# Performance work log

Measured on AMD Instinct MI355X. Metric: run time of the kernel, lower is better.

The kernel has to match this reference:

```python
import jax, jax.numpy as jnp
import numpy as np

N, L, LEADS = 512, 640, 3
COND_DIM, NUM_K, DIM_K = 1, 100, 5
FLAT = 256 * 79  # 20224, from conv stack trace


def _leaky(x):
    return jnp.where(x >= 0, x, 0.2 * x)


def _sn(w, u):
    # PyTorch spectral_norm: one power iteration (u, v detached), sigma = u^T W v
    wm = w.reshape(w.shape[0], -1)
    v = wm.T @ u
    v = v / (jnp.linalg.norm(v) + 1e-12)
    u2 = wm @ v
    u2 = u2 / (jnp.linalg.norm(u2) + 1e-12)
    u2 = jax.lax.stop_gradient(u2)
    v = jax.lax.stop_gradient(v)
    sigma = u2 @ (wm @ v)
    return w / sigma


def _conv1d(x, w, b, stride, pad):
    y = jax.lax.conv_general_dilated(
        x, w, window_strides=(stride,), padding=[(pad, pad)],
        dimension_numbers=('NCH', 'OIH', 'NCH'))
    return y + b[None, :, None]


def setup_inputs() -> dict:
    key = jax.random.key(0)
    ks = jax.random.split(key, 16)
    g = lambda k, shp, s: (jax.random.normal(k, shp, dtype=jnp.float32) * s)
    inp = {
        'ecg': jax.random.normal(ks[0], (N, L, LEADS), dtype=jnp.float32),
        'condition': jax.random.randint(ks[1], (N, 1), 0, 4),
        'w1': g(ks[2], (64, LEADS, 5), 0.2), 'b1': jnp.zeros((64,), jnp.float32),
        'u1': jax.random.normal(ks[3], (64,), dtype=jnp.float32),
        'w2': g(ks[4], (128, 64, 7), 0.05), 'b2': jnp.zeros((128,), jnp.float32),
        'u2': jax.random.normal(ks[5], (128,), dtype=jnp.float32),
        'w3': g(ks[6], (256, 128, 9), 0.03), 'b3': jnp.zeros((256,), jnp.float32),
        'u3': jax.random.normal(ks[7], (256,), dtype=jnp.float32),
        'emb': g(ks[8], (4, COND_DIM), 1.0),
        'cond_w': g(ks[9], (50, COND_DIM), 0.5), 'cond_b': jnp.zeros((50,), jnp.float32),
        'mb_w': g(ks[10], (FLAT, NUM_K * DIM_K), 0.01),
        'fc_w': g(ks[11], (1, FLAT + NUM_K + 50), 0.01), 'fc_b': jnp.zeros((1,), jnp.float32),
    }
    return inp


def reference(ecg, condition, w1, b1, u1, w2, b2, u2, w3, b3, u3,
              emb, cond_w, cond_b, mb_w, fc_w, fc_b):
    # condition embedding -> Linear(cond_dim, 50)
    cemb = emb[condition[:, 0]]                       # [N, cond_dim]
    cond = cemb @ cond_w.T + cond_b                   # [N, 50]

    x = ecg.transpose(0, 2, 1)                        # [N, 3, 640]
    x = _leaky(_conv1d(x, _sn(w1, u1), b1, 2, 4))     # [N, 64, 322]
    x = _leaky(_conv1d(x, _sn(w2, u2), b2, 2, 3))     # [N, 128, 161]
    x = _leaky(_conv1d(x, _sn(w3, u3), b3, 2, 2))     # [N, 256, 79]
    flat = x.reshape(x.shape[0], -1)                  # [N, 20224]

    # minibatch discrimination
    act = (flat @ mb_w).reshape(-1, NUM_K, DIM_K)     # [N, K, D]
    l1 = jnp.abs(act[:, None] - act[None, :]).sum(-1)  # [N, N, K]
    feats = jnp.exp(-l1).sum(axis=1)                  # [N, K]

    out = jnp.concatenate([flat, feats, cond], axis=1)
    return out @ fc_w.T + fc_b                        # [N, 1]
```

## Files before the change

kernel.cpp:

```cpp
#include <hip/hip_runtime.h>
#include <math.h>

#define NB 512
#define LIN 640
#define NLEADS 3
#define L1O 322
#define L2O 161
#define L3O 79
#define C1N 64
#define C2N 128
#define C3N 256
#define FLATSZ 20224
#define NUMK 100
#define DIMK 5
#define SPLITK 16

typedef __attribute__((ext_vector_type(8))) short short8;
typedef __attribute__((ext_vector_type(4))) float f32x4;

__device__ __forceinline__ unsigned short f2bf(float x){
  unsigned u = __builtin_bit_cast(unsigned, x);
  unsigned r = u + 0x7FFFu + ((u >> 16) & 1u);
  return (unsigned short)(r >> 16);
}
__device__ __forceinline__ float bf2f(unsigned short x){
  unsigned u = ((unsigned)x) << 16;
  return __builtin_bit_cast(float, u);
}

__device__ __forceinline__ float block_reduce_sum(float val, float* red){
#pragma unroll
  for(int off=32; off>0; off>>=1) val += __shfl_down(val, off, 64);
  int lane = threadIdx.x & 63;
  int wv = threadIdx.x >> 6;
  if(lane==0) red[wv] = val;
  __syncthreads();
  int nw = blockDim.x >> 6;
  float r = red[0];
  for(int i=1;i<nw;i++) r += red[i];
  __syncthreads();
  return r;
}

__global__ __launch_bounds__(256)
void sn_pass1(const float* __restrict__ w1, const float* __restrict__ u1,
              const float* __restrict__ w2, const float* __restrict__ u2,
              const float* __restrict__ w3, const float* __restrict__ u3,
              float* __restrict__ v_all, float* __restrict__ ss){
  __shared__ float red[4];
  int b = blockIdx.x, tid = threadIdx.x;
  const float* w; const float* u; int O, C, off, c, widx;
  if(b==0){ w=w1; u=u1; O=64;  C=15;   off=0;   c=tid;            widx=0; }
  else if(b<3){ w=w2; u=u2; O=128; C=448; off=16;  c=(b-1)*256+tid; widx=1; }
  else { w=w3; u=u3; O=256; C=1152; off=464; c=(b-3)*256+tid;      widx=2; }
  float vv = 0.f;
  if(c < C){
    for(int o=0;o<O;o+=4){
      vv += w[(o+0)*C+c]*u[o+0] + w[(o+1)*C+c]*u[o+1]
          + w[(o+2)*C+c]*u[o+2] + w[(o+3)*C+c]*u[o+3];
    }
    v_all[off + c] = vv;
  }
  float ps = (c < C) ? vv*vv : 0.f;
  float tot = block_reduce_sum(ps, red);
  if(tid==0) atomicAdd(&ss[widx], tot);
}

__global__ __launch_bounds__(256)
void sn_pass2(const float* __restrict__ w1, const float* __restrict__ w2,
              const float* __restrict__ w3, const float* __restrict__ v_all,
              float* __restrict__ Sun){
  int b = blockIdx.x, tid = threadIdx.x;
  int lane = tid & 63, wv = tid >> 6;
  const float* w; int C, off, o, widx;
  if(b < 16){ w=w1; C=15;   off=0;   o=b*4+wv;      widx=0; }
  else if(b < 48){ w=w2; C=448; off=16;  o=(b-16)*4+wv; widx=1; }
  else { w=w3; C=1152; off=464; o=(b-48)*4+wv;          widx=2; }
  float t = 0.f;
  for(int c=lane; c<C; c+=64) t += w[o*C+c]*v_all[off+c];
#pragma unroll
  for(int s=32; s>0; s>>=1) t += __shfl_down(t, s, 64);
  if(lane==0) atomicAdd(&Sun[widx], t*t);
}

__global__ void sn_final(const float* __restrict__ ss, const float* __restrict__ Sun,
                         float* __restrict__ scale){
  int tid = threadIdx.x;
  if(tid < 3){
    float inv = 1.f/(sqrtf(ss[tid])+1e-12f);
    float S = Sun[tid]*inv*inv;
    scale[tid] = (sqrtf(S)+1e-12f)/S;
  }
}

__global__ void wprep_kernel(const float* __restrict__ w1, const float* __restrict__ w2,
                             const float* __restrict__ w3, const float* __restrict__ scale,
                             unsigned short* __restrict__ w1p, unsigned short* __restrict__ w2bf,
                             unsigned short* __restrict__ w3p){
  int idx = blockIdx.x*256 + threadIdx.x;
  float s1 = scale[0], s2 = scale[1], s3 = scale[2];
  if(idx < C1N*32){
    int o = idx >> 5, kk = idx & 31;
    w1p[idx] = (kk < 15) ? f2bf(w1[o*15+kk]*s1) : 0;
  }
  if(idx < C2N*448)   w2bf[idx] = f2bf(w2[idx]*s2);
  if(idx < C3N*1152){
    int o = idx / 1152, k2 = idx - o*1152;
    int r = k2 >> 7, i = k2 & 127;
    w3p[idx] = f2bf(w3[o*1152 + i*9 + r]*s3);
  }
}

__global__ __launch_bounds__(256, 4)
void conv12_mfma(const float* __restrict__ ecg, const unsigned short* __restrict__ w1p,
                 const float* __restrict__ b1, const unsigned short* __restrict__ w2bf,
                 const float* __restrict__ b2, unsigned short* __restrict__ y2t){
  __shared__ unsigned short ysw[C1N*208];
  __shared__ unsigned short scratch[7168];
  unsigned short* B1 = scratch;
  unsigned short* As = scratch;
  unsigned short* Bs = scratch + C2N*32;
  int n = blockIdx.x, tile = blockIdx.y, tid = threadIdx.x;
  int lane = tid & 63, w = tid >> 6;
  int c0    = tile ? 189 : 0;
  int tbase = tile ? 96  : 0;
  int D     = tile ? 0   : -3;

  const float* eb = ecg + (size_t)n*LIN*NLEADS;
#pragma unroll
  for(int q=0;q<26;q++){
    int e = q*256 + tid;
    int tp = e >> 5, kk = e & 31;
    unsigned short v = 0;
    if(kk < 15){
      int i = kk/5, r = kk - i*5;
      int p = 2*(c0 + tp) - 4 + r;
      if((unsigned)p < (unsigned)LIN) v = f2bf(eb[p*NLEADS + i]);
    }
    B1[tp*32 + kk] = v;
  }
  __syncthreads();

  {
    short8 a1 = *(const short8*)(w1p + ((w*16 + (lane&15))<<5) + (lane>>4)*8);
    f32x4 zero = {0.f,0.f,0.f,0.f};
#pragma unroll
    for(int half=0; half<2; half++){
      int nt0 = half*7, ntc = half ? 6 : 7;
      f32x4 c1[7];
      for(int j=0;j<ntc;j++){
        short8 b = *(const short8*)(B1 + (((nt0+j)*16 + (lane&15))<<5) + (lane>>4)*8);
        c1[j] = __builtin_amdgcn_mfma_f32_16x16x32_bf16(a1, b, zero, 0, 0, 0);
      }
#pragma unroll
      for(int reg=0;reg<4;reg++){
        int o = w*16 + (lane>>4)*4 + reg;
        float bias = b1[o];
        for(int j=0;j<ntc;j++){
          int tp = (nt0+j)*16 + (lane&15);
          int tc = c0 + tp;
          float v = 0.f;
          if(tc < L1O){
            v = c1[j][reg] + bias;
            v = v>=0.f ? v : 0.2f*v;
          }
          ysw[o*208 + tp] = (tc < L1O) ? f2bf(v) : (unsigned short)0;
        }
      }
    }
  }

  f32x4 zero = {0.f,0.f,0.f,0.f};
  f32x4 acc[2][6];
#pragma unroll
  for(int i=0;i<2;i++)
#pragma unroll
    for(int j=0;j<6;j++) acc[i][j] = zero;

  for(int ck=0; ck<14; ck++){
    int kc = ck*32;
    __syncthreads();
    {
      const char* wb = (const char*)w2bf;
      uint4* dst = (uint4*)As;
#pragma unroll
      for(int q=0;q<2;q++){
        int f = q*256 + tid;
        int row = f >> 2, col = f & 3;
        dst[f] = *(const uint4*)(wb + row*896 + kc*2 + col*16);
      }
    }
#pragma unroll
    for(int q=0;q<12;q++){
      int e = q*256 + tid;
      int tt = e >> 5, kk = e & 31;
      int k = kc + kk;
      int i = k / 7;
      int r = k - i*7;
      int col = 2*tt + r + D;
      unsigned short v = 0;
      if((unsigned)col < 208u) v = ysw[i*208 + col];
      Bs[tt*32 + kk] = v;
    }
    __syncthreads();
    short8 a[2], b[6];
#pragma unroll
    for(int mm=0;mm<2;mm++)
      a[mm] = *(const short8*)(As + ((w*2+mm)*16 + (lane&15))*32 + (lane>>4)*8);
#pragma unroll
    for(int nt=0;nt<6;nt++)
      b[nt] = *(const short8*)(Bs + (nt*16 + (lane&15))*32 + (lane>>4)*8);
#pragma unroll
    for(int mm=0;mm<2;mm++)
#pragma unroll
      for(int nt=0;nt<6;nt++)
        acc[mm][nt] = __builtin_amdgcn_mfma_f32_16x16x32_bf16(a[mm], b[nt], acc[mm][nt], 0, 0, 0);
  }

  unsigned short* trans = ysw;
#pragma unroll
  for(int mm=0;mm<2;mm++){
#pragma unroll
    for(int reg=0;reg<4;reg++){
      int o = (w*2+mm)*16 + (lane>>4)*4 + reg;
      float bias = b2[o];
#pragma unroll
      for(int nt=0;nt<6;nt++){
        int tl = nt*16 + (lane&15);
        int t = tbase + tl;
        if(t < L2O){
          float v = acc[mm][nt][reg] + bias;
          v = v>=0.f ? v : 0.2f*v;
          trans[tl*136 + o] = f2bf(v);
        }
      }
    }
  }
  __syncthreads();
  {
    int rows = tile ? 65 : 96;
    uint4* dstg = (uint4*)(y2t + (size_t)n*20608 + tbase*128);
#pragma unroll
    for(int q=0;q<6;q++){
      int f = q*256 + tid;
      int row = f >> 4, c8 = f & 15;
      if(row < rows)
        dstg[row*16 + c8] = *(const uint4*)(trans + row*136 + c8*8);
    }
  }
}

__global__ __launch_bounds__(256, 2)
void conv3_mfma(const unsigned short* __restrict__ y2t, const unsigned short* __restrict__ w3p,
                const float* __restrict__ b3, unsigned short* __restrict__ flatbf){
  __shared__ unsigned short lds[22712];
  int n = blockIdx.x, tid = threadIdx.x;
  int lane = tid & 63, w = tid >> 6;

  if(tid < 136){
    lds[tid] = 0;
    lds[82*136 + tid] = 0;
    lds[83*136 + tid] = 0;
    lds[11424 + tid] = 0;
    lds[11424 + 81*136 + tid] = 0;
    lds[11424 + 82*136 + tid] = 0;
  }
  {
    const uint4* src = (const uint4*)(y2t + (size_t)n*20608);
#pragma unroll
    for(int q=0;q<11;q++){
      int f = q*256 + tid;
      if(f < 2576){
        int g = f >> 4, c8 = f & 15;
        int sub = g >> 1, p = g & 1;
        *(uint4*)(lds + (p ? 11424 : 0) + (sub+1)*136 + c8*8) = src[(size_t)g*16 + c8];
      }
    }
  }

  f32x4 zero = {0.f,0.f,0.f,0.f};
  f32x4 acc[4][5];
#pragma unroll
  for(int i=0;i<4;i++)
#pragma unroll
    for(int j=0;j<5;j++) acc[i][j] = zero;

  const unsigned short* wbase = w3p + ((size_t)(w*64) + (lane&15))*1152 + (lane>>4)*8;
  short8 a_cur[4];
#pragma unroll
  for(int mm=0;mm<4;mm++)
    a_cur[mm] = *(const short8*)(wbase + mm*16*1152);
  __syncthreads();

  for(int ck=0; ck<36; ck++){
    short8 a_nxt[4];
    if(ck < 35){
      int kc = (ck+1)*32;
#pragma unroll
      for(int mm=0;mm<4;mm++)
        a_nxt[mm] = *(const short8*)(wbase + mm*16*1152 + kc);
    }
    int r = ck >> 2, i0 = (ck & 3) * 32;
    int cbase = ((r & 1) ? 11424 : 0) + (r >> 1)*136 + i0 + (lane>>4)*8;
    short8 b[5];
#pragma unroll
    for(int nt=0;nt<5;nt++){
      int t = nt*16 + (lane&15);
      b[nt] = *(const short8*)(lds + cbase + t*136);
    }
#pragma unroll
    for(int mm=0;mm<4;mm++)
#pragma unroll
      for(int nt=0;nt<5;nt++)
        acc[mm][nt] = __builtin_amdgcn_mfma_f32_16x16x32_bf16(a_cur[mm], b[nt], acc[mm][nt], 0, 0, 0);
    if(ck < 35){
#pragma unroll
      for(int mm=0;mm<4;mm++) a_cur[mm] = a_nxt[mm];
    }
  }
#pragma unroll
  for(int mm=0;mm<4;mm++){
#pragma unroll
    for(int reg=0;reg<4;reg++){
      int o = w*64 + mm*16 + (lane>>4)*4 + reg;
      float bias = b3[o];
#pragma unroll
      for(int nt=0;nt<5;nt++){
        int t = nt*16 + (lane&15);
        if(t < L3O){
          float v = acc[mm][nt][reg] + bias;
          v = v>=0.f ? v : 0.2f*v;
          flatbf[(size_t)n*FLATSZ + o*L3O + t] = f2bf(v);
        }
      }
    }
  }
}

__global__ __launch_bounds__(256)
void mbw_transpose(const float* __restrict__ mbw, unsigned short* __restrict__ mbwT){
  __shared__ unsigned short tile[32][36];
  int k0 = blockIdx.x*32, n0 = blockIdx.y*32, tid = threadIdx.x;
  int r = tid >> 3, c4 = (tid & 7) * 4;
  int nbase = n0 + c4;
  if(nbase + 3 < 500){
    float4 v = *(const float4*)(mbw + (size_t)(k0+r)*500 + nbase);
    tile[r][c4+0] = f2bf(v.x);
    tile[r][c4+1] = f2bf(v.y);
    tile[r][c4+2] = f2bf(v.z);
    tile[r][c4+3] = f2bf(v.w);
  } else {
#pragma unroll
    for(int j=0;j<4;j++){
      int nn = nbase + j;
      float v = (nn < 500) ? mbw[(size_t)(k0+r)*500 + nn] : 0.f;
      tile[r][c4+j] = f2bf(v);
    }
  }
  __syncthreads();
  int nl = tid >> 3, kq = (tid & 7) * 4;
  unsigned short t0 = tile[kq+0][nl], t1 = tile[kq+1][nl];
  unsigned short t2 = tile[kq+2][nl], t3 = tile[kq+3][nl];
  uint2 p;
  p.x = (unsigned)t0 | ((unsigned)t1 << 16);
  p.y = (unsigned)t2 | ((unsigned)t3 << 16);
  *(uint2*)(mbwT + (size_t)(n0+nl)*FLATSZ + k0 + kq) = p;
}

__global__ __launch_bounds__(256)
void mb_gemm_mfma(const unsigned short* __restrict__ flatbf, const unsigned short* __restrict__ mbwT,
                  float* __restrict__ part){
  __shared__ unsigned short As[64*32];
  __shared__ unsigned short Bs[64*32];
  int tid = threadIdx.x;
  int lane = tid & 63, w = tid >> 6;
  int m0 = blockIdx.x*64, n0 = blockIdx.y*64, bz = blockIdx.z;
  int t_start = bz*39 + (bz<8 ? bz : 8);
  int t_count = 39 + (bz<8 ? 1 : 0);
  int k0 = t_start*32;
  f32x4 zero = {0.f,0.f,0.f,0.f};
  f32x4 acc[4];
#pragma unroll
  for(int i=0;i<4;i++) acc[i] = zero;
  int arow = tid >> 2, acol = (tid & 3) * 8;
  for(int t=0; t<t_count; t++, k0+=32){
    __syncthreads();
    ((uint4*)As)[tid] = *(const uint4*)(flatbf + (size_t)(m0+arow)*FLATSZ + k0 + acol);
    ((uint4*)Bs)[tid] = *(const uint4*)(mbwT  + (size_t)(n0+arow)*FLATSZ + k0 + acol);
    __syncthreads();
    short8 a = *(const short8*)(As + (w*16 + (lane&15))*32 + (lane>>4)*8);
#pragma unroll
    for(int nt=0;nt<4;nt++){
      short8 b = *(const short8*)(Bs + (nt*16 + (lane&15))*32 + (lane>>4)*8);
      acc[nt] = __builtin_amdgcn_mfma_f32_16x16x32_bf16(a, b, acc[nt], 0, 0, 0);
    }
  }
  float* po = part + (size_t)bz*NB*500;
#pragma unroll
  for(int nt=0;nt<4;nt++){
#pragma unroll
    for(int reg=0;reg<4;reg++){
      int m = m0 + w*16 + (lane>>4)*4 + reg;
      int c = n0 + nt*16 + (lane&15);
      if(c < 500) po[(size_t)m*500 + c] = acc[nt][reg];
    }
  }
}

__global__ void mb_reduce_kernel(const float* __restrict__ part, float* __restrict__ actT){
  int idx = blockIdx.x*256 + threadIdx.x;
  float s = 0.f;
#pragma unroll
  for(int z=0;z<SPLITK;z++) s += part[(size_t)z*NB*500 + idx];
  int n = idx/500, c = idx - n*500;
  actT[(size_t)c*NB + n] = s;
}

__global__ __launch_bounds__(256)
void feats_kernel(const float* __restrict__ actT, float* __restrict__ feats){
  __shared__ float ash[4][50];
  __shared__ float pred[4][4];
  int i0 = blockIdx.x*4, k0 = blockIdx.y*10;
  int tid = threadIdx.x, lane = tid & 63, wv = tid >> 6;
  if(tid < 200){
    int ii = tid/50, c = tid - ii*50;
    ash[ii][c] = actT[(size_t)(k0*5+c)*NB + i0 + ii];
  }
  __syncthreads();
  const float LOG2E = 1.4426950408889634f;
  int j1 = tid, j2 = tid + 256;
  for(int kk=0; kk<10; kk++){
    const float* r0 = actT + (size_t)(k0+kk)*5*NB;
    float xa0=r0[j1], xa1=r0[NB+j1], xa2=r0[2*NB+j1], xa3=r0[3*NB+j1], xa4=r0[4*NB+j1];
    float xb0=r0[j2], xb1=r0[NB+j2], xb2=r0[2*NB+j2], xb3=r0[3*NB+j2], xb4=r0[4*NB+j2];
    float f[4];
#pragma unroll
    for(int ii=0; ii<4; ii++){
      float a0=ash[ii][kk*5+0], a1=ash[ii][kk*5+1], a2=ash[ii][kk*5+2],
            a3=ash[ii][kk*5+3], a4=ash[ii][kk*5+4];
      float la = fabsf(xa0-a0)+fabsf(xa1-a1)+fabsf(xa2-a2)+fabsf(xa3-a3)+fabsf(xa4-a4);
      float lb = fabsf(xb0-a0)+fabsf(xb1-a1)+fabsf(xb2-a2)+fabsf(xb3-a3)+fabsf(xb4-a4);
      f[ii] = exp2f(-LOG2E*la) + exp2f(-LOG2E*lb);
    }
#pragma unroll
    for(int ii=0; ii<4; ii++){
      float v = f[ii];
#pragma unroll
      for(int s=32; s>0; s>>=1) v += __shfl_down(v, s, 64);
      if(lane==0) pred[wv][ii] = v;
    }
    __syncthreads();
    if(tid < 4){
      float v = pred[0][tid] + pred[1][tid] + pred[2][tid] + pred[3][tid];
      feats[(size_t)(i0+tid)*NUMK + k0 + kk] = v;
    }
    __syncthreads();
  }
}

__global__ void final_kernel(const unsigned short* __restrict__ flatbf, const float* __restrict__ feats,
                             const int* __restrict__ condition, const float* __restrict__ emb,
                             const float* __restrict__ cond_w, const float* __restrict__ cond_b,
                             const float* __restrict__ fc_w, const float* __restrict__ fc_b,
                             float* __restrict__ out){
  __shared__ float red[4];
  int n = blockIdx.x, tid = threadIdx.x;
  float s = 0.f;
  const unsigned short* fr = flatbf + (size_t)n*FLATSZ;
  for(int q=tid; q<FLATSZ/8; q+=256){
    uint4 u = *(const uint4*)(fr + q*8);
    float4 wa = *(const float4*)(fc_w + q*8);
    float4 wb = *(const float4*)(fc_w + q*8 + 4);
    s += bf2f((unsigned short)(u.x & 0xffff))*wa.x + bf2f((unsigned short)(u.x >> 16))*wa.y
       + bf2f((unsigned short)(u.y & 0xffff))*wa.z + bf2f((unsigned short)(u.y >> 16))*wa.w
       + bf2f((unsigned short)(u.z & 0xffff))*wb.x + bf2f((unsigned short)(u.z >> 16))*wb.y
       + bf2f((unsigned short)(u.w & 0xffff))*wb.z + bf2f((unsigned short)(u.w >> 16))*wb.w;
  }
  for(int k=tid;k<NUMK;k+=256) s += feats[n*NUMK+k]*fc_w[FLATSZ+k];
  float ce = emb[condition[n]];
  for(int j=tid;j<50;j+=256) s += (ce*cond_w[j]+cond_b[j])*fc_w[FLATSZ+NUMK+j];
  s = block_reduce_sum(s, red);
  if(tid==0) out[n] = s + fc_b[0];
}

extern "C" void kernel_launch(void* const* d_in, const int* in_sizes, int n_in,
                              void* d_out, int out_size, void* d_ws, size_t ws_size,
                              hipStream_t stream) {
  const float* ecg   = (const float*)d_in[0];
  const int*   cond  = (const int*)  d_in[1];
  const float* w1    = (const float*)d_in[2];
  const float* b1    = (const float*)d_in[3];
  const float* u1    = (const float*)d_in[4];
  const float* w2    = (const float*)d_in[5];
  const float* b2    = (const float*)d_in[6];
  const float* u2    = (const float*)d_in[7];
  const float* w3    = (const float*)d_in[8];
  const float* b3    = (const float*)d_in[9];
  const float* u3    = (const float*)d_in[10];
  const float* emb   = (const float*)d_in[11];
  const float* condw = (const float*)d_in[12];
  const float* condb = (const float*)d_in[13];
  const float* mbw   = (const float*)d_in[14];
  const float* fcw   = (const float*)d_in[15];
  const float* fcb   = (const float*)d_in[16];

  float* ws = (float*)d_ws;
  float* scale = ws;
  float* ssbuf = ws + 16;
  float* Sunbuf= ws + 24;
  float* v_all = ws + 32;
  unsigned short* w1p  = (unsigned short*)(ws + 1648);
  unsigned short* w2bf = (unsigned short*)(ws + 2672);
  unsigned short* w3p  = (unsigned short*)(ws + 31344);
  unsigned short* y2t  = (unsigned short*)(ws + 178800);
  unsigned short* mbwT = (unsigned short*)(ws + 178800);
  float* part  = ws + 5454448;
  float* actT  = ws + 9550448;
  float* feats = ws + 9806448;
  unsigned short* flatbf = (unsigned short*)(ws + 9857648);

  hipMemsetAsync((char*)d_ws + 64, 0, 64, stream);
  sn_pass1<<<8, 256, 0, stream>>>(w1,u1,w2,u2,w3,u3, v_all, ssbuf);
  sn_pass2<<<112, 256, 0, stream>>>(w1,w2,w3, v_all, Sunbuf);
  sn_final<<<1, 64, 0, stream>>>(ssbuf, Sunbuf, scale);
  wprep_kernel<<<1152, 256, 0, stream>>>(w1, w2, w3, scale, w1p, w2bf, w3p);
  conv12_mfma<<<dim3(NB,2), 256, 0, stream>>>(ecg, w1p, b1, w2bf, b2, y2t);
  conv3_mfma<<<NB, 256, 0, stream>>>(y2t, w3p, b3, flatbf);
  mbw_transpose<<<dim3(632,16), 256, 0, stream>>>(mbw, mbwT);
  mb_gemm_mfma<<<dim3(8,8,SPLITK), 256, 0, stream>>>(flatbf, mbwT, part);
  mb_reduce_kernel<<<1000, 256, 0, stream>>>(part, actT);
  feats_kernel<<<dim3(128,10), 256, 0, stream>>>(actT, feats);
  final_kernel<<<NB, 256, 0, stream>>>(flatbf, feats, cond, emb, condw, condb, fcw, fcb, (float*)d_out);
}
```

Measured before the change: 326.7 us.

## Use even/odd time-major slabs for conv2 B operand, stream weights from global

Conv1 output is now written into two time-major LDS slabs split by even and odd time step, with channels contiguous. Conv2 can then read its implicit-GEMM B fragments directly as short8 vectors, with no per-chunk im2col gather into a staging buffer. The conv2 weights are repacked tap-major in wprep and loaded per lane straight from global memory with one-step register prefetch. This removes the two barriers per K-chunk and the scalar gather loop. In exchange it adds a zero-fill pass, more LDS use, and global weight reads that are not shared across waves, which may affect occupancy.

After: 300.1 us. -8.1%, faster.

```diff
diff --git a/kernel.cpp b/kernel.cpp
--- a/kernel.cpp
+++ b/kernel.cpp
@@ -95,7 +95,7 @@
 
 __global__ void wprep_kernel(const float* __restrict__ w1, const float* __restrict__ w2,
                              const float* __restrict__ w3, const float* __restrict__ scale,
-                             unsigned short* __restrict__ w1p, unsigned short* __restrict__ w2bf,
+                             unsigned short* __restrict__ w1p, unsigned short* __restrict__ w2p,
                              unsigned short* __restrict__ w3p){
   int idx = blockIdx.x*256 + threadIdx.x;
   float s1 = scale[0], s2 = scale[1], s3 = scale[2];
@@ -103,7 +103,11 @@
     int o = idx >> 5, kk = idx & 31;
     w1p[idx] = (kk < 15) ? f2bf(w1[o*15+kk]*s1) : 0;
   }
-  if(idx < C2N*448)   w2bf[idx] = f2bf(w2[idx]*s2);
+  if(idx < C2N*448){
+    int o = idx / 448, k2 = idx - o*448;
+    int r = k2 >> 6, i = k2 & 63;
+    w2p[idx] = f2bf(w2[o*448 + i*7 + r]*s2);
+  }
   if(idx < C3N*1152){
     int o = idx / 1152, k2 = idx - o*1152;
     int r = k2 >> 7, i = k2 & 127;
@@ -113,19 +117,25 @@
 
 __global__ __launch_bounds__(256, 4)
 void conv12_mfma(const float* __restrict__ ecg, const unsigned short* __restrict__ w1p,
-                 const float* __restrict__ b1, const unsigned short* __restrict__ w2bf,
+                 const float* __restrict__ b1, const unsigned short* __restrict__ w2p,
                  const float* __restrict__ b2, unsigned short* __restrict__ y2t){
-  __shared__ unsigned short ysw[C1N*208];
-  __shared__ unsigned short scratch[7168];
-  unsigned short* B1 = scratch;
-  unsigned short* As = scratch;
-  unsigned short* Bs = scratch + C2N*32;
+  __shared__ unsigned short slabs[13600];
+  __shared__ unsigned short B1s[6656];
   int n = blockIdx.x, tile = blockIdx.y, tid = threadIdx.x;
   int lane = tid & 63, w = tid >> 6;
   int c0    = tile ? 189 : 0;
   int tbase = tile ? 96  : 0;
-  int D     = tile ? 0   : -3;
-
+  int suboff= tile ? -94 : 2;
+
+  {
+    uint4 z = {0u,0u,0u,0u};
+    uint4* zd = (uint4*)slabs;
+#pragma unroll
+    for(int q=0;q<7;q++){
+      int f = q*256 + tid;
+      if(f < 1700) zd[f] = z;
+    }
+  }
   const float* eb = ecg + (size_t)n*LIN*NLEADS;
 #pragma unroll
   for(int q=0;q<26;q++){
@@ -137,7 +147,7 @@
       int p = 2*(c0 + tp) - 4 + r;
       if((unsigned)p < (unsigned)LIN) v = f2bf(eb[p*NLEADS + i]);
     }
-    B1[tp*32 + kk] = v;
+    B1s[tp*32 + kk] = v;
   }
   __syncthreads();
 
@@ -149,7 +159,7 @@
       int nt0 = half*7, ntc = half ? 6 : 7;
       f32x4 c1[7];
       for(int j=0;j<ntc;j++){
-        short8 b = *(const short8*)(B1 + (((nt0+j)*16 + (lane&15))<<5) + (lane>>4)*8);
+        short8 b = *(const short8*)(B1s + (((nt0+j)*16 + (lane&15))<<5) + (lane>>4)*8);
         c1[j] = __builtin_amdgcn_mfma_f32_16x16x32_bf16(a1, b, zero, 0, 0, 0);
       }
 #pragma unroll
@@ -158,17 +168,18 @@
         float bias = b1[o];
         for(int j=0;j<ntc;j++){
           int tp = (nt0+j)*16 + (lane&15);
-          int tc = c0 + tp;
-          float v = 0.f;
-          if(tc < L1O){
-            v = c1[j][reg] + bias;
+          int t1 = c0 + tp;
+          int sub = (t1>>1) + suboff;
+          if(t1 < L1O && sub < 100){
+            float v = c1[j][reg] + bias;
             v = v>=0.f ? v : 0.2f*v;
+            slabs[((t1&1)?6800:0) + sub*68 + o] = f2bf(v);
           }
-          ysw[o*208 + tp] = (tc < L1O) ? f2bf(v) : (unsigned short)0;
         }
       }
     }
   }
+  __syncthreads();
 
   f32x4 zero = {0.f,0.f,0.f,0.f};
   f32x4 acc[2][6];
@@ -177,47 +188,35 @@
 #pragma unroll
     for(int j=0;j<6;j++) acc[i][j] = zero;
 
+  const unsigned short* w2base = w2p + ((size_t)(w*2*16 + (lane&15)))*448 + (lane>>4)*8;
+  short8 a_cur[2];
+  a_cur[0] = *(const short8*)(w2base);
+  a_cur[1] = *(const short8*)(w2base + 16*448);
+
   for(int ck=0; ck<14; ck++){
-    int kc = ck*32;
-    __syncthreads();
-    {
-      const char* wb = (const char*)w2bf;
-      uint4* dst = (uint4*)As;
-#pragma unroll
-      for(int q=0;q<2;q++){
-        int f = q*256 + tid;
-        int row = f >> 2, col = f & 3;
-        dst[f] = *(const uint4*)(wb + row*896 + kc*2 + col*16);
-      }
-    }
-#pragma unroll
-    for(int q=0;q<12;q++){
-      int e = q*256 + tid;
-      int tt = e >> 5, kk = e & 31;
-      int k = kc + kk;
-      int i = k / 7;
-      int r = k - i*7;
-      int col = 2*tt + r + D;
-      unsigned short v = 0;
-      if((unsigned)col < 208u) v = ysw[i*208 + col];
-      Bs[tt*32 + kk] = v;
-    }
-    __syncthreads();
-    short8 a[2], b[6];
+    short8 a_nxt[2];
+    if(ck < 13){
+      a_nxt[0] = *(const short8*)(w2base + (ck+1)*32);
+      a_nxt[1] = *(const short8*)(w2base + 16*448 + (ck+1)*32);
+    }
+    int r = ck >> 1, i0 = (ck & 1)*32;
+    int p = (r+1) & 1;
+    int m = ((r-3) - p) >> 1;
+    int base = (p?6800:0) + (m+2 + (lane&15))*68 + i0 + (lane>>4)*8;
+    short8 b[6];
+#pragma unroll
+    for(int nt=0;nt<6;nt++)
+      b[nt] = *(const short8*)(slabs + base + nt*16*68);
 #pragma unroll
     for(int mm=0;mm<2;mm++)
-      a[mm] = *(const short8*)(As + ((w*2+mm)*16 + (lane&15))*32 + (lane>>4)*8);
-#pragma unroll
-    for(int nt=0;nt<6;nt++)
-      b[nt] = *(const short8*)(Bs + (nt*16 + (lane&15))*32 + (lane>>4)*8);
-#pragma unroll
-    for(int mm=0;mm<2;mm++)
 #pragma unroll
       for(int nt=0;nt<6;nt++)
-        acc[mm][nt] = __builtin_amdgcn_mfma_f32_16x16x32_bf16(a[mm], b[nt], acc[mm][nt], 0, 0, 0);
-  }
-
-  unsigned short* trans = ysw;
+        acc[mm][nt] = __builtin_amdgcn_mfma_f32_16x16x32_bf16(a_cur[mm], b[nt], acc[mm][nt], 0, 0, 0);
+    if(ck < 13){ a_cur[0] = a_nxt[0]; a_cur[1] = a_nxt[1]; }
+  }
+
+  __syncthreads();
+  unsigned short* trans = slabs;
 #pragma unroll
   for(int mm=0;mm<2;mm++){
 #pragma unroll
@@ -510,7 +509,7 @@
   float* Sunbuf= ws + 24;
   float* v_all = ws + 32;
   unsigned short* w1p  = (unsigned short*)(ws + 1648);
-  unsigned short* w2bf = (unsigned short*)(ws + 2672);
+  unsigned short* w2p  = (unsigned short*)(ws + 2672);
   unsigned short* w3p  = (unsigned short*)(ws + 31344);
   unsigned short* y2t  = (unsigned short*)(ws + 178800);
   unsigned short* mbwT = (unsigned short*)(ws + 178800);
@@ -523,8 +522,8 @@
   sn_pass1<<<8, 256, 0, stream>>>(w1,u1,w2,u2,w3,u3, v_all, ssbuf);
   sn_pass2<<<112, 256, 0, stream>>>(w1,w2,w3, v_all, Sunbuf);
   sn_final<<<1, 64, 0, stream>>>(ssbuf, Sunbuf, scale);
-  wprep_kernel<<<1152, 256, 0, stream>>>(w1, w2, w3, scale, w1p, w2bf, w3p);
-  conv12_mfma<<<dim3(NB,2), 256, 0, stream>>>(ecg, w1p, b1, w2bf, b2, y2t);
+  wprep_kernel<<<1152, 256, 0, stream>>>(w1, w2, w3, scale, w1p, w2p, w3p);
+  conv12_mfma<<<dim3(NB,2), 256, 0, stream>>>(ecg, w1p, b1, w2p, b2, y2t);
   conv3_mfma<<<NB, 256, 0, stream>>>(y2t, w3p, b3, flatbf);
   mbw_transpose<<<dim3(632,16), 256, 0, stream>>>(mbw, mbwT);
   mb_gemm_mfma<<<dim3(8,8,SPLITK), 256, 0, stream>>>(flatbf, mbwT, part);
```
